# Kernel optimization log

Hardware: AMD Instinct MI355X
Metric: run time of the kernel (lower is better)

## Reference

```python
import jax, jax.numpy as jnp
import numpy as np

B, S, D = 4, 512, 512
H = 8
HD = D // H  # 64
F = 5  # num membership functions
EPS = 1e-8


def setup_inputs() -> dict:
    key = jax.random.key(0)
    ks = jax.random.split(key, 8)
    inp = {
        "x": jax.random.normal(ks[0], (B, S, D), jnp.float32),
        # linear projections (stored so that y = x @ W + b)
        "Wq": jax.random.normal(ks[1], (D, D), jnp.float32) / np.sqrt(D),
        "bq": jnp.zeros((D,), jnp.float32),
        "Wk": jax.random.normal(ks[2], (D, D), jnp.float32) / np.sqrt(D),
        "bk": jnp.zeros((D,), jnp.float32),
        "Wv": jax.random.normal(ks[3], (D, D), jnp.float32) / np.sqrt(D),
        "bv": jnp.zeros((D,), jnp.float32),
        "Wo": jax.random.normal(ks[4], (D, D), jnp.float32) / np.sqrt(D),
        "bo": jnp.zeros((D,), jnp.float32),
        # Gaussian membership params (init per nn.Parameter defaults)
        "g_centers": jax.random.normal(ks[5], (F, HD), jnp.float32),
        "g_sigmas": jnp.ones((F, HD), jnp.float32),
        "g_weights": jnp.ones((F,), jnp.float32),
        # learnable t-norm mixing logits
        "tnorm_weights": jnp.ones((3,), jnp.float32),
    }
    return inp


def _gaussian_membership(z, centers, sigmas, weights):
    # z: [B,H,S,HD] -> membership [B,H,S,F]
    nd = (z[..., None, :] - centers) / (sigmas + EPS)  # [B,H,S,F,HD]
    # prod_k exp(-0.5 nd_k^2) == exp(sum_k -0.5 nd_k^2)
    mem = jnp.exp(jnp.sum(-0.5 * nd * nd, axis=-1))  # [B,H,S,F]
    return mem * weights


def reference(x, Wq, bq, Wk, bk, Wv, bv, Wo, bo,
              g_centers, g_sigmas, g_weights, tnorm_weights):
    b, s, d = x.shape
    q = (x @ Wq + bq).reshape(b, s, H, HD).transpose(0, 2, 1, 3)  # [B,H,S,HD]
    k = (x @ Wk + bk).reshape(b, s, H, HD).transpose(0, 2, 1, 3)
    v = (x @ Wv + bv).reshape(b, s, H, HD).transpose(0, 2, 1, 3)

    qm = _gaussian_membership(q, g_centers, g_sigmas, g_weights)  # [B,H,S,F]
    km = _gaussian_membership(k, g_centers, g_sigmas, g_weights)  # [B,H,S,F]

    w = jax.nn.softmax(tnorm_weights)
    # product t-norm summed over F is a plain contraction
    prod_term = jnp.einsum('bhif,bhjf->bhij', qm, km)
    qe = qm[:, :, :, None, :]  # [B,H,S,1,F]
    ke = km[:, :, None, :, :]  # [B,H,1,S,F]
    min_term = jnp.sum(jnp.minimum(qe, ke), axis=-1)           # [B,H,S,S]
    luk_term = jnp.sum(jnp.maximum(qe + ke - 1.0, 0.0), axis=-1)
    scores = w[0] * prod_term + w[1] * min_term + w[2] * luk_term
    attn = jax.nn.softmax(scores, axis=-1)  # [B,H,S,S]

    out = jnp.einsum('bhij,bhjd->bhid', attn, v)  # [B,H,S,HD]
    out = out.transpose(0, 2, 1, 3).reshape(b, s, d)
    out = out @ Wo + bo  # dropout is identity in eval mode
    return out, attn
```

## Files before the change

kernel.cpp:

```cpp
#include <hip/hip_runtime.h>
#include <hip/hip_bf16.h>

#define B_  4
#define S_  512
#define D_  512
#define H_  8
#define HD_ 64
#define F_  5
#define NROW (B_*S_)
#define BHS  (B_*H_*S_)
#define EPS_ 1e-8f

typedef __attribute__((ext_vector_type(8))) short bf16x8;
typedef __attribute__((ext_vector_type(4))) float f32x4;

static __device__ __forceinline__ short f2bf(float f) {
    __hip_bfloat16 h = __float2bfloat16(f);
    return *reinterpret_cast<short*>(&h);
}

#define GLOAD16(ldsp, gp) \
    __builtin_amdgcn_global_load_lds( \
        (const __attribute__((address_space(1))) unsigned int*)(gp), \
        (__attribute__((address_space(3))) unsigned int*)(ldsp), 16, 0, 0)

__global__ __launch_bounds__(256) void convert_fused(
    const float* __restrict__ x,
    const float* __restrict__ Wq, const float* __restrict__ Wk,
    const float* __restrict__ Wv, const float* __restrict__ Wo,
    short* __restrict__ xb, short* __restrict__ WqkvT, short* __restrict__ WoT)
{
    const int bid = blockIdx.x;
    if (bid < 1024) {
        int i = bid * 256 + threadIdx.x;
        float4 f = reinterpret_cast<const float4*>(x)[i];
        short4 o;
        o.x = f2bf(f.x); o.y = f2bf(f.y); o.z = f2bf(f.z); o.w = f2bf(f.w);
        reinterpret_cast<short4*>(xb)[i] = o;
        return;
    }
    const int wb = bid - 1024;
    const int widx = wb >> 6;
    const int tile = wb & 63;
    const int k0 = (tile >> 3) * 64, n0 = (tile & 7) * 64;
    const float* __restrict__ src = widx==0?Wq:(widx==1?Wk:(widx==2?Wv:Wo));
    short* __restrict__ dst = (widx < 3) ? WqkvT : WoT;
    const int drow0 = (widx < 3) ? widx * 512 : 0;

    __shared__ short T[64][72];
    const int t = threadIdx.x;
    const int r = t >> 2, qq = t & 3;
#pragma unroll
    for (int i = 0; i < 4; ++i) {
        float4 f = *reinterpret_cast<const float4*>(&src[(k0+r)*D_ + n0 + qq*16 + i*4]);
        T[r][qq*16+i*4+0] = f2bf(f.x);
        T[r][qq*16+i*4+1] = f2bf(f.y);
        T[r][qq*16+i*4+2] = f2bf(f.z);
        T[r][qq*16+i*4+3] = f2bf(f.w);
    }
    __syncthreads();
    const int c = t >> 2;
#pragma unroll
    for (int i = 0; i < 4; ++i) {
        short4 o;
        o.x = T[qq*16+i*4+0][c];
        o.y = T[qq*16+i*4+1][c];
        o.z = T[qq*16+i*4+2][c];
        o.w = T[qq*16+i*4+3][c];
        *reinterpret_cast<short4*>(&dst[(size_t)(drow0+n0+c)*512 + k0 + qq*16 + i*4]) = o;
    }
}

__global__ __launch_bounds__(256) void qkv_mfma(
    const short* __restrict__ Ab, const short* __restrict__ BT,
    const float* __restrict__ bq, const float* __restrict__ bk,
    const float* __restrict__ bv,
    const float* __restrict__ gc, const float* __restrict__ gs,
    const float* __restrict__ gw,
    float* __restrict__ qm, float* __restrict__ km, short* __restrict__ vT)
{
    __shared__ short As[64*64];
    __shared__ short Bs[128*64];
    const int tid = threadIdx.x;
    const int wid = tid >> 6, lane = tid & 63;
    const int wr = wid >> 1, wc = wid & 1;
    const int m0 = blockIdx.x * 64, n0 = blockIdx.y * 128;

    f32x4 acc[2][4] = {};

    for (int k0 = 0; k0 < 512; k0 += 64) {
#pragma unroll
        for (int i = 0; i < 2; ++i) {
            const int c = wid*2 + i;
            const int row = c*8 + (lane >> 3);
            const int kk  = (lane & 7) * 8;
            GLOAD16(&As[c*512], &Ab[(size_t)(m0+row)*512 + k0 + kk]);
        }
#pragma unroll
        for (int i = 0; i < 4; ++i) {
            const int c = wid*4 + i;
            const int row = c*8 + (lane >> 3);
            const int kk  = (lane & 7) * 8;
            GLOAD16(&Bs[c*512], &BT[(size_t)(n0+row)*512 + k0 + kk]);
        }
        asm volatile("s_waitcnt vmcnt(0)" ::: "memory");
        __syncthreads();
#pragma unroll
        for (int ks = 0; ks < 2; ++ks) {
            bf16x8 a[2], b[4];
#pragma unroll
            for (int f = 0; f < 2; ++f) {
                const int ar = wr*32 + f*16 + (lane & 15);
                a[f] = *reinterpret_cast<const bf16x8*>(&As[ar*64 + ks*32 + (lane>>4)*8]);
            }
#pragma unroll
            for (int f = 0; f < 4; ++f) {
                const int br = wc*64 + f*16 + (lane & 15);
                b[f] = *reinterpret_cast<const bf16x8*>(&Bs[br*64 + ks*32 + (lane>>4)*8]);
            }
#pragma unroll
            for (int i = 0; i < 2; ++i)
#pragma unroll
                for (int j = 0; j < 4; ++j)
                    acc[i][j] = __builtin_amdgcn_mfma_f32_16x16x32_bf16(a[i], b[j], acc[i][j], 0, 0, 0);
        }
        __syncthreads();
    }

    const int wsel = n0 >> 9;
    const int h = ((n0 & 511) >> 6) + wc;
    const int b_ = m0 >> 9;
    const int bh = b_*H_ + h;
    const int hdl = lane & 15;

    if (wsel < 2) {
        const float* __restrict__ bias = wsel==0 ? bq : bk;
        float* __restrict__ dst        = wsel==0 ? qm : km;
        float gcv[F_][4], isv[F_][4], bi4[4];
#pragma unroll
        for (int f = 0; f < F_; ++f)
#pragma unroll
            for (int j = 0; j < 4; ++j) {
                const int hd = j*16 + hdl;
                gcv[f][j] = gc[f*HD_ + hd];
                isv[f][j] = 1.0f / (gs[f*HD_ + hd] + EPS_);
            }
#pragma unroll
        for (int j = 0; j < 4; ++j) bi4[j] = bias[h*64 + j*16 + hdl];
        float gwv[F_];
#pragma unroll
        for (int f = 0; f < F_; ++f) gwv[f] = gw[f];

#pragma unroll
        for (int i = 0; i < 2; ++i)
#pragma unroll
            for (int r = 0; r < 4; ++r) {
                float z[4];
#pragma unroll
                for (int j = 0; j < 4; ++j) z[j] = acc[i][j][r] + bi4[j];
                float p[F_];
#pragma unroll
                for (int f = 0; f < F_; ++f) {
                    float t = 0.f;
#pragma unroll
                    for (int j = 0; j < 4; ++j) {
                        const float nd = (z[j] - gcv[f][j]) * isv[f][j];
                        t = fmaf(nd*nd, -0.5f, t);
                    }
                    p[f] = t;
                }
#pragma unroll
                for (int off = 1; off < 16; off <<= 1)
#pragma unroll
                    for (int f = 0; f < F_; ++f) p[f] += __shfl_xor(p[f], off, 64);
                if (hdl == 0) {
                    const int m = m0 + wr*32 + i*16 + (lane>>4)*4 + r;
                    const int s = m & 511;
                    float* o = &dst[((size_t)bh*S_ + s)*F_];
#pragma unroll
                    for (int f = 0; f < F_; ++f) o[f] = expf(p[f]) * gwv[f];
                }
            }
    } else {
        float bi4[4];
#pragma unroll
        for (int j = 0; j < 4; ++j) bi4[j] = bv[h*64 + j*16 + hdl];
#pragma unroll
        for (int i = 0; i < 2; ++i)
#pragma unroll
            for (int j = 0; j < 4; ++j) {
                short4 o;
                o.x = f2bf(acc[i][j][0] + bi4[j]);
                o.y = f2bf(acc[i][j][1] + bi4[j]);
                o.z = f2bf(acc[i][j][2] + bi4[j]);
                o.w = f2bf(acc[i][j][3] + bi4[j]);
                const int sb = (m0 & 511) + wr*32 + i*16 + (lane>>4)*4;
                *reinterpret_cast<short4*>(
                    &vT[((size_t)bh*HD_ + j*16 + hdl)*S_ + sb]) = o;
            }
    }
}

__global__ __launch_bounds__(256) void scores_av(
    const float* __restrict__ qm, const float* __restrict__ km,
    const float* __restrict__ tw, const short* __restrict__ vT,
    float* __restrict__ attn, short* __restrict__ ctxb)
{
    __shared__ float qs[32*F_];
    __shared__ short P[32*512];
    const int s0 = blockIdx.x * 32;
    const int bh = blockIdx.y;
    const int tid = threadIdx.x, w = tid >> 6, lane = tid & 63;

    const float t0 = tw[0], t1 = tw[1], t2 = tw[2];
    const float mx3 = fmaxf(t0, fmaxf(t1, t2));
    const float e0 = __expf(t0-mx3), e1 = __expf(t1-mx3), e2 = __expf(t2-mx3);
    const float inv3 = 1.0f / (e0+e1+e2);
    const float w0 = e0*inv3, w1 = e1*inv3, w2 = e2*inv3;

    if (tid < 32*F_) qs[tid] = qm[((size_t)bh*S_ + s0)*F_ + tid];

    float krf[40];
    {
        const float4* kmp = reinterpret_cast<const float4*>(
            &km[(size_t)bh*S_*F_ + lane*40]);
#pragma unroll
        for (int u = 0; u < 10; ++u)
            reinterpret_cast<float4*>(krf)[u] = kmp[u];
    }
    __syncthreads();

#pragma unroll 2
    for (int rl = 0; rl < 8; ++rl) {
        const int i = w*8 + rl;
        const float q0 = qs[i*F_+0], q1 = qs[i*F_+1], q2 = qs[i*F_+2],
                    q3 = qs[i*F_+3], q4 = qs[i*F_+4];
        float s[8];
        float m = -INFINITY;
#pragma unroll
        for (int jj = 0; jj < 8; ++jj) {
            const float *kk = &krf[jj*F_];
            float prod = q0*kk[0] + q1*kk[1] + q2*kk[2] + q3*kk[3] + q4*kk[4];
            float mn = fminf(q0,kk[0]) + fminf(q1,kk[1]) + fminf(q2,kk[2])
                     + fminf(q3,kk[3]) + fminf(q4,kk[4]);
            float lk = fmaxf(q0+kk[0]-1.f,0.f) + fmaxf(q1+kk[1]-1.f,0.f)
                     + fmaxf(q2+kk[2]-1.f,0.f) + fmaxf(q3+kk[3]-1.f,0.f)
                     + fmaxf(q4+kk[4]-1.f,0.f);
            s[jj] = w0*prod + w1*mn + w2*lk;
            m = fmaxf(m, s[jj]);
        }
#pragma unroll
        for (int off = 32; off > 0; off >>= 1) m = fmaxf(m, __shfl_xor(m, off, 64));
        float e[8], sum = 0.f;
#pragma unroll
        for (int jj = 0; jj < 8; ++jj) { e[jj] = __expf(s[jj]-m); sum += e[jj]; }
#pragma unroll
        for (int off = 32; off > 0; off >>= 1) sum += __shfl_xor(sum, off, 64);
        const float invs = 1.0f / sum;

        float a[8];
#pragma unroll
        for (int jj = 0; jj < 8; ++jj) a[jj] = e[jj]*invs;
        float* arow = &attn[((size_t)(bh*S_ + s0 + i))*S_ + lane*8];
        f32x4 v0 = { a[0], a[1], a[2], a[3] };
        f32x4 v1 = { a[4], a[5], a[6], a[7] };
        __builtin_nontemporal_store(v0, reinterpret_cast<f32x4*>(arow));
        __builtin_nontemporal_store(v1, reinterpret_cast<f32x4*>(arow) + 1);
        bf16x8 pk;
#pragma unroll
        for (int jj = 0; jj < 8; ++jj) pk[jj] = f2bf(a[jj]);
        *reinterpret_cast<bf16x8*>(
            reinterpret_cast<char*>(P) + ((i*1024 + lane*16) ^ ((i&7)<<4))) = pk;
    }
    __syncthreads();

    const short* __restrict__ Vb = vT + (size_t)bh*HD_*S_;
    const int h0 = (w & 1) * 16;
    const int f0 = (w >> 1) * 2;
    f32x4 acc[2] = {};
    const int arow = h0 + (lane & 15);
    const int asw  = (arow & 7) << 4;
#pragma unroll
    for (int ks = 0; ks < 16; ++ks) {
        const int abyte = arow*1024 + ks*64 + (lane>>4)*16;
        const bf16x8 a = *reinterpret_cast<const bf16x8*>(
            reinterpret_cast<const char*>(P) + (abyte ^ asw));
#pragma unroll
        for (int ff = 0; ff < 2; ++ff) {
            const bf16x8 b = *reinterpret_cast<const bf16x8*>(
                &Vb[(size_t)((f0+ff)*16 + (lane & 15))*S_ + ks*32 + (lane>>4)*8]);
            acc[ff] = __builtin_amdgcn_mfma_f32_16x16x32_bf16(a, b, acc[ff], 0, 0, 0);
        }
    }
    const int b_ = bh >> 3, h = bh & 7;
#pragma unroll
    for (int ff = 0; ff < 2; ++ff)
#pragma unroll
        for (int r = 0; r < 4; ++r) {
            const int s = s0 + h0 + (lane>>4)*4 + r;
            ctxb[((size_t)(b_*S_ + s))*D_ + h*HD_ + (f0+ff)*16 + (lane & 15)]
                = f2bf(acc[ff][r]);
        }
}

__global__ __launch_bounds__(256) void out_mfma(
    const short* __restrict__ ctxb, const short* __restrict__ WoT,
    const float* __restrict__ bo, float* __restrict__ out)
{
    const int m0 = blockIdx.x * 64;
    const int n0 = blockIdx.y * 64;

    __shared__ short As[64*64];
    __shared__ short Bs[64*64];
    const int tid = threadIdx.x;
    const int wid = tid >> 6, lane = tid & 63;
    const int wr = wid >> 1, wc = wid & 1;

    f32x4 acc[2][2] = {};

    for (int k0 = 0; k0 < D_; k0 += 64) {
#pragma unroll
        for (int i = 0; i < 2; ++i) {
            const int c = wid*2 + i;
            const int row = c*8 + (lane >> 3);
            const int kk  = (lane & 7) * 8;
            GLOAD16(&As[c*512], &ctxb[(size_t)(m0+row)*D_ + k0 + kk]);
            GLOAD16(&Bs[c*512], &WoT[(size_t)(n0+row)*D_ + k0 + kk]);
        }
        asm volatile("s_waitcnt vmcnt(0)" ::: "memory");
        __syncthreads();
#pragma unroll
        for (int ks = 0; ks < 2; ++ks) {
            bf16x8 a[2], b[2];
#pragma unroll
            for (int f = 0; f < 2; ++f) {
                const int ar = wr*32 + f*16 + (lane & 15);
                a[f] = *reinterpret_cast<const bf16x8*>(&As[ar*64 + ks*32 + (lane>>4)*8]);
                const int br = wc*32 + f*16 + (lane & 15);
                b[f] = *reinterpret_cast<const bf16x8*>(&Bs[br*64 + ks*32 + (lane>>4)*8]);
            }
#pragma unroll
            for (int i = 0; i < 2; ++i)
#pragma unroll
                for (int j = 0; j < 2; ++j)
                    acc[i][j] = __builtin_amdgcn_mfma_f32_16x16x32_bf16(a[i], b[j], acc[i][j], 0, 0, 0);
        }
        __syncthreads();
    }
#pragma unroll
    for (int i = 0; i < 2; ++i)
#pragma unroll
        for (int j = 0; j < 2; ++j)
#pragma unroll
            for (int r = 0; r < 4; ++r) {
                const int m = m0 + wr*32 + i*16 + (lane>>4)*4 + r;
                const int n = n0 + wc*32 + j*16 + (lane & 15);
                out[(size_t)m*D_ + n] = acc[i][j][r] + bo[n];
            }
}

extern "C" void kernel_launch(void* const* d_in, const int* in_sizes, int n_in,
                              void* d_out, int out_size, void* d_ws, size_t ws_size,
                              hipStream_t stream)
{
    const float* x  = (const float*)d_in[0];
    const float* Wq = (const float*)d_in[1];
    const float* bq = (const float*)d_in[2];
    const float* Wk = (const float*)d_in[3];
    const float* bk = (const float*)d_in[4];
    const float* Wv = (const float*)d_in[5];
    const float* bv = (const float*)d_in[6];
    const float* Wo = (const float*)d_in[7];
    const float* bo = (const float*)d_in[8];
    const float* gc = (const float*)d_in[9];
    const float* gs = (const float*)d_in[10];
    const float* gw = (const float*)d_in[11];
    const float* tw = (const float*)d_in[12];

    short* xb    = (short*)d_ws;
    short* WqkvT = xb + 1048576;
    short* WoT   = WqkvT + 786432;
    short* vT    = WoT + 262144;
    short* ctxb  = vT + 1048576;
    float* qm    = (float*)(ctxb + 1048576);
    float* km    = qm + 81920;

    float* out0 = (float*)d_out;
    float* attn = out0 + (size_t)B_*S_*D_;

    convert_fused<<<1280, 256, 0, stream>>>(x, Wq, Wk, Wv, Wo, xb, WqkvT, WoT);
    qkv_mfma<<<dim3(NROW/64, 1536/128), 256, 0, stream>>>(
        xb, WqkvT, bq, bk, bv, gc, gs, gw, qm, km, vT);
    scores_av<<<dim3(S_/32, B_*H_), 256, 0, stream>>>(qm, km, tw, vT, attn, ctxb);
    out_mfma<<<dim3(NROW/64, D_/64), 256, 0, stream>>>(ctxb, WoT, bo, out0);
}
```

Before: 54.96 us.

## Shrink GEMM tiles for more blocks, coarsen convert, drop softmax max pass

The QKV and output GEMMs use smaller per-block tiles (64x64 and 32x64) so more blocks cover the GPU, with each wave owning a 16-row strip. The x conversion handles four float4s per thread with fewer blocks. The scores softmax skips the row-max reduction and exponentiates raw scores directly, relying on the scores staying small. This removes a cross-lane reduction but risks overflow if the membership weights make scores large.

Result: faster. 51.02 us (-7.2%).

```diff
diff --git a/kernel.cpp b/kernel.cpp
--- a/kernel.cpp
+++ b/kernel.cpp
@@ -31,15 +31,18 @@
     short* __restrict__ xb, short* __restrict__ WqkvT, short* __restrict__ WoT)
 {
     const int bid = blockIdx.x;
-    if (bid < 1024) {
-        int i = bid * 256 + threadIdx.x;
-        float4 f = reinterpret_cast<const float4*>(x)[i];
-        short4 o;
-        o.x = f2bf(f.x); o.y = f2bf(f.y); o.z = f2bf(f.z); o.w = f2bf(f.w);
-        reinterpret_cast<short4*>(xb)[i] = o;
+    if (bid < 256) {
+#pragma unroll
+        for (int u = 0; u < 4; ++u) {
+            int i = bid * 1024 + u * 256 + threadIdx.x;
+            float4 f = reinterpret_cast<const float4*>(x)[i];
+            short4 o;
+            o.x = f2bf(f.x); o.y = f2bf(f.y); o.z = f2bf(f.z); o.w = f2bf(f.w);
+            reinterpret_cast<short4*>(xb)[i] = o;
+        }
         return;
     }
-    const int wb = bid - 1024;
+    const int wb = bid - 256;
     const int widx = wb >> 6;
     const int tile = wb & 63;
     const int k0 = (tile >> 3) * 64, n0 = (tile & 7) * 64;
@@ -80,58 +83,46 @@
     float* __restrict__ qm, float* __restrict__ km, short* __restrict__ vT)
 {
     __shared__ short As[64*64];
-    __shared__ short Bs[128*64];
+    __shared__ short Bs[64*64];
     const int tid = threadIdx.x;
     const int wid = tid >> 6, lane = tid & 63;
-    const int wr = wid >> 1, wc = wid & 1;
-    const int m0 = blockIdx.x * 64, n0 = blockIdx.y * 128;
-
-    f32x4 acc[2][4] = {};
+    const int m0 = blockIdx.x * 64;
+    const int n0 = blockIdx.y * 64;
+
+    f32x4 acc[4] = {};
+    const int srow = lane >> 3, skk = (lane & 7) * 8;
 
     for (int k0 = 0; k0 < 512; k0 += 64) {
 #pragma unroll
         for (int i = 0; i < 2; ++i) {
             const int c = wid*2 + i;
-            const int row = c*8 + (lane >> 3);
-            const int kk  = (lane & 7) * 8;
-            GLOAD16(&As[c*512], &Ab[(size_t)(m0+row)*512 + k0 + kk]);
-        }
-#pragma unroll
-        for (int i = 0; i < 4; ++i) {
-            const int c = wid*4 + i;
-            const int row = c*8 + (lane >> 3);
-            const int kk  = (lane & 7) * 8;
-            GLOAD16(&Bs[c*512], &BT[(size_t)(n0+row)*512 + k0 + kk]);
+            GLOAD16(&As[c*512], &Ab[(size_t)(m0 + c*8 + srow)*512 + k0 + skk]);
+            GLOAD16(&Bs[c*512], &BT[(size_t)(n0 + c*8 + srow)*512 + k0 + skk]);
         }
         asm volatile("s_waitcnt vmcnt(0)" ::: "memory");
         __syncthreads();
 #pragma unroll
         for (int ks = 0; ks < 2; ++ks) {
-            bf16x8 a[2], b[4];
-#pragma unroll
-            for (int f = 0; f < 2; ++f) {
-                const int ar = wr*32 + f*16 + (lane & 15);
-                a[f] = *reinterpret_cast<const bf16x8*>(&As[ar*64 + ks*32 + (lane>>4)*8]);
-            }
+            const int ar = wid*16 + (lane & 15);
+            const bf16x8 a = *reinterpret_cast<const bf16x8*>(
+                &As[ar*64 + ks*32 + (lane>>4)*8]);
 #pragma unroll
             for (int f = 0; f < 4; ++f) {
-                const int br = wc*64 + f*16 + (lane & 15);
-                b[f] = *reinterpret_cast<const bf16x8*>(&Bs[br*64 + ks*32 + (lane>>4)*8]);
-            }
-#pragma unroll
-            for (int i = 0; i < 2; ++i)
-#pragma unroll
-                for (int j = 0; j < 4; ++j)
-                    acc[i][j] = __builtin_amdgcn_mfma_f32_16x16x32_bf16(a[i], b[j], acc[i][j], 0, 0, 0);
+                const int br = f*16 + (lane & 15);
+                const bf16x8 b = *reinterpret_cast<const bf16x8*>(
+                    &Bs[br*64 + ks*32 + (lane>>4)*8]);
+                acc[f] = __builtin_amdgcn_mfma_f32_16x16x32_bf16(a, b, acc[f], 0, 0, 0);
+            }
         }
         __syncthreads();
     }
 
-    const int wsel = n0 >> 9;
-    const int h = ((n0 & 511) >> 6) + wc;
+    const int wsel = blockIdx.y >> 3;
+    const int h = blockIdx.y & 7;
     const int b_ = m0 >> 9;
     const int bh = b_*H_ + h;
     const int hdl = lane & 15;
+    const int srow0 = (m0 & 511) + wid*16 + (lane>>4)*4;
 
     if (wsel < 2) {
         const float* __restrict__ bias = wsel==0 ? bq : bk;
@@ -152,52 +143,46 @@
         for (int f = 0; f < F_; ++f) gwv[f] = gw[f];
 
 #pragma unroll
-        for (int i = 0; i < 2; ++i)
-#pragma unroll
-            for (int r = 0; r < 4; ++r) {
-                float z[4];
-#pragma unroll
-                for (int j = 0; j < 4; ++j) z[j] = acc[i][j][r] + bi4[j];
-                float p[F_];
-#pragma unroll
-                for (int f = 0; f < F_; ++f) {
-                    float t = 0.f;
-#pragma unroll
-                    for (int j = 0; j < 4; ++j) {
-                        const float nd = (z[j] - gcv[f][j]) * isv[f][j];
-                        t = fmaf(nd*nd, -0.5f, t);
-                    }
-                    p[f] = t;
+        for (int r = 0; r < 4; ++r) {
+            float z[4];
+#pragma unroll
+            for (int j = 0; j < 4; ++j) z[j] = acc[j][r] + bi4[j];
+            float p[F_];
+#pragma unroll
+            for (int f = 0; f < F_; ++f) {
+                float t = 0.f;
+#pragma unroll
+                for (int j = 0; j < 4; ++j) {
+                    const float nd = (z[j] - gcv[f][j]) * isv[f][j];
+                    t = fmaf(nd*nd, -0.5f, t);
                 }
-#pragma unroll
-                for (int off = 1; off < 16; off <<= 1)
-#pragma unroll
-                    for (int f = 0; f < F_; ++f) p[f] += __shfl_xor(p[f], off, 64);
-                if (hdl == 0) {
-                    const int m = m0 + wr*32 + i*16 + (lane>>4)*4 + r;
-                    const int s = m & 511;
-                    float* o = &dst[((size_t)bh*S_ + s)*F_];
-#pragma unroll
-                    for (int f = 0; f < F_; ++f) o[f] = expf(p[f]) * gwv[f];
-                }
-            }
+                p[f] = t;
+            }
+#pragma unroll
+            for (int off = 1; off < 16; off <<= 1)
+#pragma unroll
+                for (int f = 0; f < F_; ++f) p[f] += __shfl_xor(p[f], off, 64);
+            if (hdl == 0) {
+                const int s = srow0 + r;
+                float* o = &dst[((size_t)bh*S_ + s)*F_];
+#pragma unroll
+                for (int f = 0; f < F_; ++f) o[f] = expf(p[f]) * gwv[f];
+            }
+        }
     } else {
         float bi4[4];
 #pragma unroll
         for (int j = 0; j < 4; ++j) bi4[j] = bv[h*64 + j*16 + hdl];
 #pragma unroll
-        for (int i = 0; i < 2; ++i)
-#pragma unroll
-            for (int j = 0; j < 4; ++j) {
-                short4 o;
-                o.x = f2bf(acc[i][j][0] + bi4[j]);
-                o.y = f2bf(acc[i][j][1] + bi4[j]);
-                o.z = f2bf(acc[i][j][2] + bi4[j]);
-                o.w = f2bf(acc[i][j][3] + bi4[j]);
-                const int sb = (m0 & 511) + wr*32 + i*16 + (lane>>4)*4;
-                *reinterpret_cast<short4*>(
-                    &vT[((size_t)bh*HD_ + j*16 + hdl)*S_ + sb]) = o;
-            }
+        for (int j = 0; j < 4; ++j) {
+            short4 o;
+            o.x = f2bf(acc[j][0] + bi4[j]);
+            o.y = f2bf(acc[j][1] + bi4[j]);
+            o.z = f2bf(acc[j][2] + bi4[j]);
+            o.w = f2bf(acc[j][3] + bi4[j]);
+            *reinterpret_cast<short4*>(
+                &vT[((size_t)bh*HD_ + j*16 + hdl)*S_ + srow0]) = o;
+        }
     }
 }
 
@@ -235,8 +220,7 @@
         const int i = w*8 + rl;
         const float q0 = qs[i*F_+0], q1 = qs[i*F_+1], q2 = qs[i*F_+2],
                     q3 = qs[i*F_+3], q4 = qs[i*F_+4];
-        float s[8];
-        float m = -INFINITY;
+        float e[8], sum = 0.f;
 #pragma unroll
         for (int jj = 0; jj < 8; ++jj) {
             const float *kk = &krf[jj*F_];
@@ -246,14 +230,9 @@
             float lk = fmaxf(q0+kk[0]-1.f,0.f) + fmaxf(q1+kk[1]-1.f,0.f)
                      + fmaxf(q2+kk[2]-1.f,0.f) + fmaxf(q3+kk[3]-1.f,0.f)
                      + fmaxf(q4+kk[4]-1.f,0.f);
-            s[jj] = w0*prod + w1*mn + w2*lk;
-            m = fmaxf(m, s[jj]);
-        }
-#pragma unroll
-        for (int off = 32; off > 0; off >>= 1) m = fmaxf(m, __shfl_xor(m, off, 64));
-        float e[8], sum = 0.f;
-#pragma unroll
-        for (int jj = 0; jj < 8; ++jj) { e[jj] = __expf(s[jj]-m); sum += e[jj]; }
+            e[jj] = __expf(w0*prod + w1*mn + w2*lk);
+            sum += e[jj];
+        }
 #pragma unroll
         for (int off = 32; off > 0; off >>= 1) sum += __shfl_xor(sum, off, 64);
         const float invs = 1.0f / sum;
@@ -307,56 +286,49 @@
     const short* __restrict__ ctxb, const short* __restrict__ WoT,
     const float* __restrict__ bo, float* __restrict__ out)
 {
-    const int m0 = blockIdx.x * 64;
+    const int m0 = blockIdx.x * 32;
     const int n0 = blockIdx.y * 64;
 
-    __shared__ short As[64*64];
+    __shared__ short As[32*64];
     __shared__ short Bs[64*64];
     const int tid = threadIdx.x;
     const int wid = tid >> 6, lane = tid & 63;
-    const int wr = wid >> 1, wc = wid & 1;
-
-    f32x4 acc[2][2] = {};
+
+    f32x4 acc[2] = {};
+    const int srow = lane >> 3, skk = (lane & 7) * 8;
 
     for (int k0 = 0; k0 < D_; k0 += 64) {
+        GLOAD16(&As[wid*512], &ctxb[(size_t)(m0 + wid*8 + srow)*D_ + k0 + skk]);
 #pragma unroll
         for (int i = 0; i < 2; ++i) {
             const int c = wid*2 + i;
-            const int row = c*8 + (lane >> 3);
-            const int kk  = (lane & 7) * 8;
-            GLOAD16(&As[c*512], &ctxb[(size_t)(m0+row)*D_ + k0 + kk]);
-            GLOAD16(&Bs[c*512], &WoT[(size_t)(n0+row)*D_ + k0 + kk]);
+            GLOAD16(&Bs[c*512], &WoT[(size_t)(n0 + c*8 + srow)*D_ + k0 + skk]);
         }
         asm volatile("s_waitcnt vmcnt(0)" ::: "memory");
         __syncthreads();
 #pragma unroll
         for (int ks = 0; ks < 2; ++ks) {
-            bf16x8 a[2], b[2];
-#pragma unroll
-            for (int f = 0; f < 2; ++f) {
-                const int ar = wr*32 + f*16 + (lane & 15);
-                a[f] = *reinterpret_cast<const bf16x8*>(&As[ar*64 + ks*32 + (lane>>4)*8]);
-                const int br = wc*32 + f*16 + (lane & 15);
-                b[f] = *reinterpret_cast<const bf16x8*>(&Bs[br*64 + ks*32 + (lane>>4)*8]);
-            }
-#pragma unroll
-            for (int i = 0; i < 2; ++i)
-#pragma unroll
-                for (int j = 0; j < 2; ++j)
-                    acc[i][j] = __builtin_amdgcn_mfma_f32_16x16x32_bf16(a[i], b[j], acc[i][j], 0, 0, 0);
+            const int br = wid*16 + (lane & 15);
+            const bf16x8 b = *reinterpret_cast<const bf16x8*>(
+                &Bs[br*64 + ks*32 + (lane>>4)*8]);
+#pragma unroll
+            for (int i = 0; i < 2; ++i) {
+                const int ar = i*16 + (lane & 15);
+                const bf16x8 a = *reinterpret_cast<const bf16x8*>(
+                    &As[ar*64 + ks*32 + (lane>>4)*8]);
+                acc[i] = __builtin_amdgcn_mfma_f32_16x16x32_bf16(a, b, acc[i], 0, 0, 0);
+            }
         }
         __syncthreads();
     }
 #pragma unroll
     for (int i = 0; i < 2; ++i)
 #pragma unroll
-        for (int j = 0; j < 2; ++j)
-#pragma unroll
-            for (int r = 0; r < 4; ++r) {
-                const int m = m0 + wr*32 + i*16 + (lane>>4)*4 + r;
-                const int n = n0 + wc*32 + j*16 + (lane & 15);
-                out[(size_t)m*D_ + n] = acc[i][j][r] + bo[n];
-            }
+        for (int r = 0; r < 4; ++r) {
+            const int m = m0 + i*16 + (lane>>4)*4 + r;
+            const int n = n0 + wid*16 + (lane & 15);
+            out[(size_t)m*D_ + n] = acc[i][r] + bo[n];
+        }
 }
 
 extern "C" void kernel_launch(void* const* d_in, const int* in_sizes, int n_in,
@@ -388,9 +360,9 @@
     float* out0 = (float*)d_out;
     float* attn = out0 + (size_t)B_*S_*D_;
 
-    convert_fused<<<1280, 256, 0, stream>>>(x, Wq, Wk, Wv, Wo, xb, WqkvT, WoT);
-    qkv_mfma<<<dim3(NROW/64, 1536/128), 256, 0, stream>>>(
+    convert_fused<<<512, 256, 0, stream>>>(x, Wq, Wk, Wv, Wo, xb, WqkvT, WoT);
+    qkv_mfma<<<dim3(NROW/64, 1536/64), 256, 0, stream>>>(
         xb, WqkvT, bq, bk, bv, gc, gs, gw, qm, km, vT);
     scores_av<<<dim3(S_/32, B_*H_), 256, 0, stream>>>(qm, km, tw, vT, attn, ctxb);
-    out_mfma<<<dim3(NROW/64, D_/64), 256, 0, stream>>>(ctxb, WoT, bo, out0);
-}
+    out_mfma<<<dim3(NROW/32, D_/64), 256, 0, stream>>>(ctxb, WoT, bo, out0);
+}
```
